# Performance work log

Hardware: AMD Instinct MI355X
Metric: run time of the kernel (lower is better)

## Reference

```python
import jax, jax.numpy as jnp
import numpy as np

B, C, H, W = 8, 512, 32, 32
MID = 64  # in_ch // k = 512 // 8
BN_EPS = 1e-5


def conv1x1(x, Wt, b):
    # x: [B,C,H,W], Wt: [O,C], b: [O]
    return jnp.einsum('bchw,oc->bohw', x, Wt) + b[None, :, None, None]


def batchnorm(x, gamma, beta):
    # train-mode BN: batch statistics over (B,H,W)
    mu = jnp.mean(x, axis=(0, 2, 3), keepdims=True)
    var = jnp.var(x, axis=(0, 2, 3), keepdims=True)
    xn = (x - mu) * jax.lax.rsqrt(var + BN_EPS)
    return xn * gamma[None, :, None, None] + beta[None, :, None, None]


def setup_inputs() -> dict:
    key = jax.random.key(0)
    ks = jax.random.split(key, 8)
    scale = 1.0 / np.sqrt(C)
    x = jax.random.normal(ks[0], (B, C, H, W), dtype=jnp.float32)
    Wf = jax.random.normal(ks[1], (MID, C), dtype=jnp.float32) * scale
    Wg = jax.random.normal(ks[2], (MID, C), dtype=jnp.float32) * scale
    Wh = jax.random.normal(ks[3], (MID, C), dtype=jnp.float32) * scale
    Wv = jax.random.normal(ks[4], (C, MID), dtype=jnp.float32) * (1.0 / np.sqrt(MID))
    return {
        'x': x,
        'Wf': Wf, 'bf': jnp.zeros((MID,), jnp.float32),
        'gamma_f': jnp.ones((MID,), jnp.float32), 'beta_f': jnp.zeros((MID,), jnp.float32),
        'Wg': Wg, 'bg': jnp.zeros((MID,), jnp.float32),
        'gamma_g': jnp.ones((MID,), jnp.float32), 'beta_g': jnp.zeros((MID,), jnp.float32),
        'Wh': Wh, 'bh': jnp.zeros((MID,), jnp.float32),
        'Wv': Wv, 'bv': jnp.zeros((C,), jnp.float32),
    }


def reference(x, Wf, bf, gamma_f, beta_f, Wg, bg, gamma_g, beta_g, Wh, bh, Wv, bv):
    b, c, h, w = x.shape
    hw = h * w
    f_x = jax.nn.relu(batchnorm(conv1x1(x, Wf, bf), gamma_f, beta_f)).reshape(b, MID, hw)
    g_x = jax.nn.relu(batchnorm(conv1x1(x, Wg, bg), gamma_g, beta_g)).reshape(b, MID, hw)
    h_x = conv1x1(x, Wh, bh).reshape(b, MID, hw)
    # z = f_x^T @ g_x : [B, HW, HW]
    z = jnp.einsum('bcn,bcm->bnm', f_x, g_x)
    # spectral normalization by the top singular value
    S = jnp.linalg.svd(z, compute_uv=False)  # sorted descending
    sigma = S[:, 0][:, None, None]
    attn = z / sigma
    # attn @ h_x^T -> [B, HW, MID], then permute to [B, MID, H, W]
    z2 = jnp.einsum('bnm,bcm->bcn', attn, h_x).reshape(b, MID, h, w)
    return conv1x1(z2, Wv, bv) + x
```

## Files before the change

kernel.cpp:

```cpp
#include <hip/hip_runtime.h>

#define B_   8
#define C_   512
#define HW_  1024
#define NCOL (B_*HW_)
#define NROWS 192
#define EPS  1e-5f
#define NCHUNK 32

#define YOFF   0
#define YSZ    (NROWS*NCOL)
#define SPOFF  (YOFF+YSZ)
#define SPSZ   256
#define SP2OFF (SPOFF+SPSZ)
#define SP2SZ  (256*256)
#define CPOFF  (SP2OFF+SP2SZ)
#define CPSZ   (24*NCHUNK*4096)
#define CMOFF  (CPOFF+CPSZ)
#define CMSZ   (24*4096)
#define ISOFF  (CMOFF+CMSZ)
#define UOFF   (ISOFF+16)

typedef unsigned short u16;
typedef __attribute__((ext_vector_type(8))) short short8;
typedef __attribute__((ext_vector_type(4))) float f32x4;

__device__ __forceinline__ u16 f2bf(float f) {
  unsigned u = __float_as_uint(f);
  unsigned r = u + 0x7fffu + ((u >> 16) & 1u);
  return (u16)(r >> 16);
}
__device__ __forceinline__ float bf2f(u16 h) {
  return __uint_as_float(((unsigned)h) << 16);
}
__device__ __forceinline__ void wsplit8(const float* p, short8& hi, short8& lo) {
  #pragma unroll
  for (int i = 0; i < 8; ++i) {
    const float v = p[i];
    const unsigned u = __float_as_uint(v);
    const u16 h = (u16)(u >> 16);
    const float r = v - __uint_as_float(((unsigned)h) << 16);
    const u16 l = (u16)(__float_as_uint(r) >> 16);
    hi[i] = (short)h; lo[i] = (short)l;
  }
}
#define MFMA_B16(a,b,c) __builtin_amdgcn_mfma_f32_16x16x32_bf16(a,b,c,0,0,0)

#define FMA16(a, bb) \
  acc[0][0]+=a.x*bb.x; acc[0][1]+=a.x*bb.y; acc[0][2]+=a.x*bb.z; acc[0][3]+=a.x*bb.w; \
  acc[1][0]+=a.y*bb.x; acc[1][1]+=a.y*bb.y; acc[1][2]+=a.y*bb.z; acc[1][3]+=a.y*bb.w; \
  acc[2][0]+=a.z*bb.x; acc[2][1]+=a.z*bb.y; acc[2][2]+=a.z*bb.z; acc[2][3]+=a.z*bb.w; \
  acc[3][0]+=a.w*bb.x; acc[3][1]+=a.w*bb.y; acc[3][2]+=a.w*bb.z; acc[3][3]+=a.w*bb.w;

__global__ __launch_bounds__(256) void k_conv(
    const float* __restrict__ x,
    const float* __restrict__ Wf, const float* __restrict__ Wg, const float* __restrict__ Wh,
    const float* __restrict__ bf, const float* __restrict__ bg, const float* __restrict__ bh,
    float* __restrict__ ws)
{
  __shared__ u16 Xh[8*32*8];
  __shared__ u16 Xl[8*32*8];
  const int bid = blockIdx.x;
  const int n0  = bid * 32;
  const int b   = n0 >> 10;
  const int hw0 = n0 & 1023;
  const int t   = threadIdx.x;
  const int lane = t & 63;
  const int wid  = t >> 6;
  const int wrow0 = wid * 48;
  const int cst = t & 31, kg2 = t >> 5;
  const int lm = lane & 15, lk = lane >> 4;

  const float* Wrow[3];
  #pragma unroll
  for (int mt = 0; mt < 3; ++mt) {
    const int row = wrow0 + mt*16 + lm;
    Wrow[mt] = (row < 64)  ? Wf + (size_t)row*C_
             : (row < 128) ? Wg + (size_t)(row-64)*C_
             :               Wh + (size_t)(row-128)*C_;
  }

  f32x4 acc[3][2];
  #pragma unroll
  for (int i=0;i<3;++i) { acc[i][0]=(f32x4)0.f; acc[i][1]=(f32x4)0.f; }

  for (int j = 0; j < 8; ++j) {
    const int kk = j*64;
    __syncthreads();
    {
      const float* xp = x + ((size_t)(b*C_ + kk + kg2*8))*HW_ + hw0 + cst;
      u16 hb[8], lb[8];
      #pragma unroll
      for (int i=0;i<8;++i) {
        const float v = xp[(size_t)i*HW_];
        hb[i] = f2bf(v); lb[i] = f2bf(v - bf2f(hb[i]));
      }
      uint4 ph, pl;
      ph.x=(unsigned)hb[0]|((unsigned)hb[1]<<16); ph.y=(unsigned)hb[2]|((unsigned)hb[3]<<16);
      ph.z=(unsigned)hb[4]|((unsigned)hb[5]<<16); ph.w=(unsigned)hb[6]|((unsigned)hb[7]<<16);
      pl.x=(unsigned)lb[0]|((unsigned)lb[1]<<16); pl.y=(unsigned)lb[2]|((unsigned)lb[3]<<16);
      pl.z=(unsigned)lb[4]|((unsigned)lb[5]<<16); pl.w=(unsigned)lb[6]|((unsigned)lb[7]<<16);
      *reinterpret_cast<uint4*>(&Xh[(kg2*32+cst)*8]) = ph;
      *reinterpret_cast<uint4*>(&Xl[(kg2*32+cst)*8]) = pl;
    }
    __syncthreads();
    #pragma unroll
    for (int kb = 0; kb < 2; ++kb) {
      short8 bhf[2], blf[2];
      #pragma unroll
      for (int nt = 0; nt < 2; ++nt) {
        const int col = nt*16 + lm;
        const int idx = ((kb*4 + lk)*32 + col)*8;
        bhf[nt] = *reinterpret_cast<const short8*>(&Xh[idx]);
        blf[nt] = *reinterpret_cast<const short8*>(&Xl[idx]);
      }
      #pragma unroll
      for (int mt = 0; mt < 3; ++mt) {
        float wv[8];
        *reinterpret_cast<float4*>(&wv[0]) = *reinterpret_cast<const float4*>(&Wrow[mt][kk + kb*32 + lk*8]);
        *reinterpret_cast<float4*>(&wv[4]) = *reinterpret_cast<const float4*>(&Wrow[mt][kk + kb*32 + lk*8 + 4]);
        short8 ah, al;
        wsplit8(wv, ah, al);
        #pragma unroll
        for (int nt = 0; nt < 2; ++nt) {
          acc[mt][nt] = MFMA_B16(ah, bhf[nt], acc[mt][nt]);
          acc[mt][nt] = MFMA_B16(al, bhf[nt], acc[mt][nt]);
          acc[mt][nt] = MFMA_B16(ah, blf[nt], acc[mt][nt]);
        }
      }
    }
  }
  #pragma unroll
  for (int mt = 0; mt < 3; ++mt) {
    const int rbase = wrow0 + mt*16;
    const float* bp = (rbase < 64) ? bf : (rbase < 128) ? bg : bh;
    const int rloc0 = (rbase & 63) + lk*4;
    #pragma unroll
    for (int r = 0; r < 4; ++r) {
      const int row = rbase + lk*4 + r;
      const float bi = bp[rloc0 + r];
      const float y0 = acc[mt][0][r] + bi;
      const float y1 = acc[mt][1][r] + bi;
      ws[YOFF + (size_t)row*NCOL + n0 + lm]      = y0;
      ws[YOFF + (size_t)row*NCOL + n0 + 16 + lm] = y1;
      if (rbase < 128) {
        float s  = y0 + y1;
        float s2 = y0*y0 + y1*y1;
        #pragma unroll
        for (int off = 1; off < 16; off <<= 1) {
          s  += __shfl_xor(s,  off);
          s2 += __shfl_xor(s2, off);
        }
        if (lm == 0) {
          ws[SP2OFF + bid*256 + row*2 + 0] = s;
          ws[SP2OFF + bid*256 + row*2 + 1] = s2;
        }
      }
    }
  }
}

__global__ __launch_bounds__(256) void k_cpart(
    const float* __restrict__ gamma_f, const float* __restrict__ beta_f,
    const float* __restrict__ gamma_g, const float* __restrict__ beta_g,
    float* __restrict__ ws)
{
  __shared__ u16 Sh[3][64][40];
  __shared__ u16 Sl[3][64][40];
  __shared__ float tot[256];
  __shared__ float scs[128], sfs[128];
  const int chunk = blockIdx.x, b = blockIdx.y;
  const int t = threadIdx.x;

  {
    float s = 0.f;
    const float* sp = ws + SP2OFF + t;
    #pragma unroll 8
    for (int blk = 0; blk < 256; ++blk) s += sp[blk*256];
    tot[t] = s;
  }
  __syncthreads();
  if (t < 128) {
    const float s = tot[t*2], s2 = tot[t*2+1];
    const float mean = s*(1.0f/NCOL);
    const float var  = s2*(1.0f/NCOL) - mean*mean;
    const float g  = (t < 64) ? gamma_f[t] : gamma_g[t-64];
    const float be = (t < 64) ? beta_f[t]  : beta_g[t-64];
    const float sc = g * rsqrtf(var + EPS);
    const float sf = be - mean*sc;
    scs[t] = sc; sfs[t] = sf;
    if (chunk == 0 && b == 0) {
      const int jj = (t < 64) ? t : t + 64;
      ws[SPOFF + jj]      = sc;
      ws[SPOFF + jj + 64] = sf;
    }
  }
  __syncthreads();

  const int bcol0 = b*1024 + chunk*32;
  for (int q = t; q < 1536; q += 256) {
    const int mm = q >> 9, rem = q & 511;
    const int r = rem >> 3, c4 = (rem & 7) * 4;
    const float4 v = *reinterpret_cast<const float4*>(
        &ws[YOFF + (size_t)(mm*64 + r)*NCOL + bcol0 + c4]);
    float v0, v1, v2, v3;
    if (mm < 2) {
      const float sc = scs[mm*64 + r], sf = sfs[mm*64 + r];
      v0 = fmaxf(sc*v.x+sf, 0.f); v1 = fmaxf(sc*v.y+sf, 0.f);
      v2 = fmaxf(sc*v.z+sf, 0.f); v3 = fmaxf(sc*v.w+sf, 0.f);
    } else { v0=v.x; v1=v.y; v2=v.z; v3=v.w; }
    const u16 h0=f2bf(v0), h1=f2bf(v1), h2=f2bf(v2), h3=f2bf(v3);
    uint2 ph; ph.x=(unsigned)h0|((unsigned)h1<<16); ph.y=(unsigned)h2|((unsigned)h3<<16);
    uint2 pl;
    pl.x=(unsigned)f2bf(v0-bf2f(h0)) | ((unsigned)f2bf(v1-bf2f(h1))<<16);
    pl.y=(unsigned)f2bf(v2-bf2f(h2)) | ((unsigned)f2bf(v3-bf2f(h3))<<16);
    *reinterpret_cast<uint2*>(&Sh[mm][r][c4]) = ph;
    *reinterpret_cast<uint2*>(&Sl[mm][r][c4]) = pl;
  }
  __syncthreads();
  {
    const int lane = t & 63, wid = t >> 6;
    const int lm = lane & 15, lk = lane >> 4;
    const int mt0 = (wid >> 1)*2, nt0 = (wid & 1)*2;
    const int ko = lk*8;
    short8 ah[3][2], al[3][2];
    #pragma unroll
    for (int m = 0; m < 3; ++m)
      #pragma unroll
      for (int mi = 0; mi < 2; ++mi) {
        const int row = (mt0+mi)*16 + lm;
        ah[m][mi] = *reinterpret_cast<const short8*>(&Sh[m][row][ko]);
        al[m][mi] = *reinterpret_cast<const short8*>(&Sl[m][row][ko]);
      }
    short8 bhf[2][2], blf[2][2];
    #pragma unroll
    for (int m = 0; m < 2; ++m)
      #pragma unroll
      for (int ni = 0; ni < 2; ++ni) {
        const int row = (nt0+ni)*16 + lm;
        bhf[m][ni] = *reinterpret_cast<const short8*>(&Sh[m][row][ko]);
        blf[m][ni] = *reinterpret_cast<const short8*>(&Sl[m][row][ko]);
      }
    f32x4 acc2[3][2][2];
    #pragma unroll
    for (int p=0;p<3;++p) for (int i=0;i<2;++i) for (int j=0;j<2;++j) acc2[p][i][j]=(f32x4)0.f;
    #pragma unroll
    for (int p = 0; p < 3; ++p) {
      const int am = p;
      const int bm = (p==0) ? 0 : 1;
      #pragma unroll
      for (int mi = 0; mi < 2; ++mi)
        #pragma unroll
        for (int ni = 0; ni < 2; ++ni) {
          acc2[p][mi][ni] = MFMA_B16(ah[am][mi], bhf[bm][ni], acc2[p][mi][ni]);
          acc2[p][mi][ni] = MFMA_B16(al[am][mi], bhf[bm][ni], acc2[p][mi][ni]);
          acc2[p][mi][ni] = MFMA_B16(ah[am][mi], blf[bm][ni], acc2[p][mi][ni]);
        }
    }
    float* cp = ws + CPOFF;
    #pragma unroll
    for (int p = 0; p < 3; ++p) {
      float* base = cp + ((size_t)((b*3+p)*NCHUNK + chunk))*4096;
      #pragma unroll
      for (int mi = 0; mi < 2; ++mi)
        #pragma unroll
        for (int ni = 0; ni < 2; ++ni) {
          const int col = (nt0+ni)*16 + lm;
          #pragma unroll
          for (int r = 0; r < 4; ++r) {
            const int row = (mt0+mi)*16 + lk*4 + r;
            base[(size_t)row*64 + col] = acc2[p][mi][ni][r];
          }
        }
    }
  }
}

__global__ __launch_bounds__(256) void k_creduce(float* __restrict__ ws)
{
  const int m = blockIdx.y;
  const int q = blockIdx.x*256 + threadIdx.x;
  const float4* src = reinterpret_cast<const float4*>(ws + CPOFF) + (size_t)m*NCHUNK*1024;
  float4 s = {0.f,0.f,0.f,0.f};
  #pragma unroll 8
  for (int ch = 0; ch < NCHUNK; ++ch) {
    const float4 p = src[(size_t)ch*1024 + q];
    s.x+=p.x; s.y+=p.y; s.z+=p.z; s.w+=p.w;
  }
  *(reinterpret_cast<float4*>(ws + CMOFF) + (size_t)m*1024 + q) = s;
}

__global__ __launch_bounds__(256) void k_su(const float* __restrict__ Wv, float* __restrict__ ws)
{
  __shared__ float smA[64][64];
  __shared__ float smB[64][64];
  const int bid = blockIdx.x;
  const int t = threadIdx.x;
  if (bid < 64) {
    const int b = bid >> 3, rt = bid & 7;
    const float* T = ws + CMOFF + (size_t)(b*3+2)*4096;
    for (int q = t; q < 1024; q += 256)
      *(reinterpret_cast<float4*>(&smB[0][0]) + q) = *(reinterpret_cast<const float4*>(T) + q);
    for (int q = t; q < 1024; q += 256) {
      const int row = q >> 4;
      const int c4  = (q & 15) * 4;
      const float4 wv = *reinterpret_cast<const float4*>(&Wv[(size_t)(rt*64+row)*64 + c4]);
      smA[c4+0][row]=wv.x; smA[c4+1][row]=wv.y; smA[c4+2][row]=wv.z; smA[c4+3][row]=wv.w;
    }
    __syncthreads();
    const int ti = t >> 4, tj = t & 15;
    float acc[4][4] = {};
    #pragma unroll
    for (int c = 0; c < 64; ++c) {
      const float4 a  = *reinterpret_cast<const float4*>(&smA[c][ti*4]);
      const float4 bb = *reinterpret_cast<const float4*>(&smB[c][tj*4]);
      FMA16(a, bb)
    }
    #pragma unroll
    for (int i = 0; i < 4; ++i) {
      float4 o; o.x = acc[i][0]; o.y = acc[i][1]; o.z = acc[i][2]; o.w = acc[i][3];
      *reinterpret_cast<float4*>(&ws[UOFF + ((size_t)b*512 + rt*64 + ti*4+i)*64 + tj*4]) = o;
    }
  } else {
    const int b = bid - 64;
    float* vsh = &smA[0][0];
    float* ush = &smA[1][0];
    const float* Cf = ws + CMOFF + (size_t)(b*3+0)*4096;
    const float* Cg = ws + CMOFF + (size_t)(b*3+1)*4096;
    float cfr[64], cgr[64];
    if (t < 64) {
      #pragma unroll
      for (int k4 = 0; k4 < 16; ++k4) {
        const float4 fa = *reinterpret_cast<const float4*>(&Cf[t*64 + k4*4]);
        const float4 fc = *reinterpret_cast<const float4*>(&Cg[t*64 + k4*4]);
        cfr[k4*4+0]=fa.x; cfr[k4*4+1]=fa.y; cfr[k4*4+2]=fa.z; cfr[k4*4+3]=fa.w;
        cgr[k4*4+0]=fc.x; cgr[k4*4+1]=fc.y; cgr[k4*4+2]=fc.z; cgr[k4*4+3]=fc.w;
      }
    }
    float vloc = 0.125f;
    if (t < 64) vsh[t] = vloc;
    __syncthreads();
    const int NIT = 16;
    float lambda = 0.f;
    for (int it = 0; it <= NIT; ++it) {
      if (t < 64) {
        float u0=0.f,u1=0.f,u2=0.f,u3=0.f;
        #pragma unroll
        for (int j4 = 0; j4 < 16; ++j4) {
          const float4 vq = *reinterpret_cast<const float4*>(&vsh[j4*4]);
          u0 += cfr[j4*4+0]*vq.x; u1 += cfr[j4*4+1]*vq.y;
          u2 += cfr[j4*4+2]*vq.z; u3 += cfr[j4*4+3]*vq.w;
        }
        ush[t] = (u0+u1)+(u2+u3);
      }
      __syncthreads();
      float w = 0.f;
      if (t < 64) {
        float w0=0.f,w1=0.f,w2=0.f,w3=0.f;
        #pragma unroll
        for (int j4 = 0; j4 < 16; ++j4) {
          const float4 uq = *reinterpret_cast<const float4*>(&ush[j4*4]);
          w0 += cgr[j4*4+0]*uq.x; w1 += cgr[j4*4+1]*uq.y;
          w2 += cgr[j4*4+2]*uq.z; w3 += cgr[j4*4+3]*uq.w;
        }
        w = (w0+w1)+(w2+w3);
      }
      if (it == NIT) {
        if (t < 64) {
          float num = vloc * w;
          #pragma unroll
          for (int off = 32; off > 0; off >>= 1) num += __shfl_xor(num, off);
          lambda = num;
        }
      } else {
        if (t < 64) {
          float n2 = w*w;
          #pragma unroll
          for (int off = 32; off > 0; off >>= 1) n2 += __shfl_xor(n2, off);
          const float rn = rsqrtf(fmaxf(n2, 1e-30f));
          vloc = w * rn;
        }
        __syncthreads();
        if (t < 64) vsh[t] = vloc;
        __syncthreads();
      }
    }
    if (t == 0) ws[ISOFF + b] = rsqrtf(fmaxf(lambda, 1e-30f));
  }
}

__global__ __launch_bounds__(256) void k_final(
    const float* __restrict__ x, const float* __restrict__ bv,
    float* __restrict__ out, const float* __restrict__ ws)
{
  __shared__ float Ut[64][64];
  __shared__ float Fl[64][64];
  __shared__ float scF[64], sfF[64];
  const int nt = blockIdx.x, ot = blockIdx.y, b = blockIdx.z;
  const int t = threadIdx.x;
  if (t < 64) {
    scF[t] = ws[SPOFF + t];
    sfF[t] = ws[SPOFF + 64 + t];
  }
  for (int q = t; q < 1024; q += 256) {
    const int row = q >> 4, k4 = (q & 15)*4;
    const float4 uv = *reinterpret_cast<const float4*>(
        &ws[UOFF + ((size_t)b*512 + ot*64 + row)*64 + k4]);
    Ut[k4+0][row]=uv.x; Ut[k4+1][row]=uv.y; Ut[k4+2][row]=uv.z; Ut[k4+3][row]=uv.w;
  }
  for (int q = t; q < 1024; q += 256) {
    const int k = q >> 4, c4 = (q & 15)*4;
    const float4 yv = *reinterpret_cast<const float4*>(
        &ws[YOFF + (size_t)k*NCOL + b*1024 + nt*64 + c4]);
    Fl[k][c4+0]=yv.x; Fl[k][c4+1]=yv.y; Fl[k][c4+2]=yv.z; Fl[k][c4+3]=yv.w;
  }
  __syncthreads();
  for (int q = t; q < 1024; q += 256) {
    const int k = q >> 4, c4 = (q & 15)*4;
    const float s = scF[k], f = sfF[k];
    Fl[k][c4+0]=fmaxf(s*Fl[k][c4+0]+f,0.f); Fl[k][c4+1]=fmaxf(s*Fl[k][c4+1]+f,0.f);
    Fl[k][c4+2]=fmaxf(s*Fl[k][c4+2]+f,0.f); Fl[k][c4+3]=fmaxf(s*Fl[k][c4+3]+f,0.f);
  }
  __syncthreads();
  const float isig = ws[ISOFF + b];
  const int ti = t >> 4, tj = t & 15;
  float acc[4][4] = {};
  #pragma unroll
  for (int k = 0; k < 64; ++k) {
    const float4 a  = *reinterpret_cast<const float4*>(&Ut[k][ti*4]);
    const float4 bb = *reinterpret_cast<const float4*>(&Fl[k][tj*4]);
    FMA16(a, bb)
  }
  #pragma unroll
  for (int i = 0; i < 4; ++i) {
    const int oc = ot*64 + ti*4 + i;
    const float bvv = bv[oc];
    const size_t base = ((size_t)b*C_ + oc)*HW_ + nt*64 + tj*4;
    const float4 xv = *reinterpret_cast<const float4*>(&x[base]);
    float4 o;
    o.x = acc[i][0]*isig+bvv+xv.x; o.y = acc[i][1]*isig+bvv+xv.y;
    o.z = acc[i][2]*isig+bvv+xv.z; o.w = acc[i][3]*isig+bvv+xv.w;
    *reinterpret_cast<float4*>(&out[base]) = o;
  }
}

extern "C" void kernel_launch(void* const* d_in, const int* in_sizes, int n_in,
                              void* d_out, int out_size, void* d_ws, size_t ws_size,
                              hipStream_t stream) {
  (void)in_sizes; (void)n_in; (void)out_size; (void)ws_size;
  const float* x       = (const float*)d_in[0];
  const float* Wf      = (const float*)d_in[1];
  const float* bf      = (const float*)d_in[2];
  const float* gamma_f = (const float*)d_in[3];
  const float* beta_f  = (const float*)d_in[4];
  const float* Wg      = (const float*)d_in[5];
  const float* bg      = (const float*)d_in[6];
  const float* gamma_g = (const float*)d_in[7];
  const float* beta_g  = (const float*)d_in[8];
  const float* Wh      = (const float*)d_in[9];
  const float* bh      = (const float*)d_in[10];
  const float* Wv      = (const float*)d_in[11];
  const float* bv      = (const float*)d_in[12];
  float* out = (float*)d_out;
  float* ws  = (float*)d_ws;

  k_conv   <<<256,             256, 0, stream>>>(x, Wf, Wg, Wh, bf, bg, bh, ws);
  k_cpart  <<<dim3(NCHUNK,8),  256, 0, stream>>>(gamma_f, beta_f, gamma_g, beta_g, ws);
  k_creduce<<<dim3(4,24),      256, 0, stream>>>(ws);
  k_su     <<<72,              256, 0, stream>>>(Wv, ws);
  k_final  <<<dim3(16,8,8),    256, 0, stream>>>(x, bv, out, ws);
}
```

Baseline: 86.58 us.

## Pre-split conv weights once, prefetch x into registers, fold chunk reduction into k_su

A new k_prep kernel splits the f/g/h weights into bf16 hi/lo arrays once, so k_conv loads ready bf16 fragments instead of redoing the split in every block. k_conv now loads all 64 x values per thread into registers up front, so global loads are issued early rather than inside the loop. The k_creduce launch is removed, and k_su sums the 32 partial chunks itself into padded shared memory. This trades one extra small launch for one fewer launch, at the cost of more register pressure in k_conv and redundant partial-sum reads across the 8 row-tile blocks per batch in k_su.

```diff
diff --git a/kernel.cpp b/kernel.cpp
--- a/kernel.cpp
+++ b/kernel.cpp
@@ -14,11 +14,11 @@
 #define SPSZ   256
 #define SP2OFF (SPOFF+SPSZ)
 #define SP2SZ  (256*256)
-#define CPOFF  (SP2OFF+SP2SZ)
+#define WOFF   (SP2OFF+SP2SZ)
+#define WSZ    98304
+#define CPOFF  (WOFF+WSZ)
 #define CPSZ   (24*NCHUNK*4096)
-#define CMOFF  (CPOFF+CPSZ)
-#define CMSZ   (24*4096)
-#define ISOFF  (CMOFF+CMSZ)
+#define ISOFF  (CPOFF+CPSZ)
 #define UOFF   (ISOFF+16)
 
 typedef unsigned short u16;
@@ -32,17 +32,6 @@
 }
 __device__ __forceinline__ float bf2f(u16 h) {
   return __uint_as_float(((unsigned)h) << 16);
-}
-__device__ __forceinline__ void wsplit8(const float* p, short8& hi, short8& lo) {
-  #pragma unroll
-  for (int i = 0; i < 8; ++i) {
-    const float v = p[i];
-    const unsigned u = __float_as_uint(v);
-    const u16 h = (u16)(u >> 16);
-    const float r = v - __uint_as_float(((unsigned)h) << 16);
-    const u16 l = (u16)(__float_as_uint(r) >> 16);
-    hi[i] = (short)h; lo[i] = (short)l;
-  }
 }
 #define MFMA_B16(a,b,c) __builtin_amdgcn_mfma_f32_16x16x32_bf16(a,b,c,0,0,0)
 
@@ -52,14 +41,36 @@
   acc[2][0]+=a.z*bb.x; acc[2][1]+=a.z*bb.y; acc[2][2]+=a.z*bb.z; acc[2][3]+=a.z*bb.w; \
   acc[3][0]+=a.w*bb.x; acc[3][1]+=a.w*bb.y; acc[3][2]+=a.w*bb.z; acc[3][3]+=a.w*bb.w;
 
+__global__ __launch_bounds__(256) void k_prep(
+    const float* __restrict__ Wf, const float* __restrict__ Wg,
+    const float* __restrict__ Wh, float* __restrict__ ws)
+{
+  u16* Whi = (u16*)(ws + WOFF);
+  u16* Wlo = Whi + NROWS*C_;
+  const int e4 = blockIdx.x*256 + threadIdx.x;
+  const int e  = e4*4;
+  const int row = e >> 9, k = e & 511;
+  const float* src = (row < 64) ? &Wf[row*C_ + k]
+                   : (row < 128) ? &Wg[(row-64)*C_ + k]
+                   : &Wh[(row-128)*C_ + k];
+  const float4 v = *reinterpret_cast<const float4*>(src);
+  u16 h0=f2bf(v.x), h1=f2bf(v.y), h2=f2bf(v.z), h3=f2bf(v.w);
+  u16 l0=f2bf(v.x-bf2f(h0)), l1=f2bf(v.y-bf2f(h1)), l2=f2bf(v.z-bf2f(h2)), l3=f2bf(v.w-bf2f(h3));
+  uint2 ph; ph.x = (unsigned)h0 | ((unsigned)h1<<16); ph.y = (unsigned)h2 | ((unsigned)h3<<16);
+  uint2 pl; pl.x = (unsigned)l0 | ((unsigned)l1<<16); pl.y = (unsigned)l2 | ((unsigned)l3<<16);
+  *reinterpret_cast<uint2*>(&Whi[e]) = ph;
+  *reinterpret_cast<uint2*>(&Wlo[e]) = pl;
+}
+
 __global__ __launch_bounds__(256) void k_conv(
     const float* __restrict__ x,
-    const float* __restrict__ Wf, const float* __restrict__ Wg, const float* __restrict__ Wh,
     const float* __restrict__ bf, const float* __restrict__ bg, const float* __restrict__ bh,
     float* __restrict__ ws)
 {
   __shared__ u16 Xh[8*32*8];
   __shared__ u16 Xl[8*32*8];
+  const u16* Whi = (const u16*)(ws + WOFF);
+  const u16* Wlo = Whi + NROWS*C_;
   const int bid = blockIdx.x;
   const int n0  = bid * 32;
   const int b   = n0 >> 10;
@@ -71,28 +82,29 @@
   const int cst = t & 31, kg2 = t >> 5;
   const int lm = lane & 15, lk = lane >> 4;
 
-  const float* Wrow[3];
-  #pragma unroll
-  for (int mt = 0; mt < 3; ++mt) {
-    const int row = wrow0 + mt*16 + lm;
-    Wrow[mt] = (row < 64)  ? Wf + (size_t)row*C_
-             : (row < 128) ? Wg + (size_t)(row-64)*C_
-             :               Wh + (size_t)(row-128)*C_;
+  float xr[64];
+  {
+    const float* xp = x + ((size_t)(b*C_ + kg2*8))*HW_ + hw0 + cst;
+    #pragma unroll
+    for (int j = 0; j < 8; ++j)
+      #pragma unroll
+      for (int i = 0; i < 8; ++i)
+        xr[j*8+i] = xp[(size_t)(j*64 + i)*HW_];
   }
 
   f32x4 acc[3][2];
   #pragma unroll
   for (int i=0;i<3;++i) { acc[i][0]=(f32x4)0.f; acc[i][1]=(f32x4)0.f; }
 
+  #pragma unroll
   for (int j = 0; j < 8; ++j) {
     const int kk = j*64;
     __syncthreads();
     {
-      const float* xp = x + ((size_t)(b*C_ + kk + kg2*8))*HW_ + hw0 + cst;
       u16 hb[8], lb[8];
       #pragma unroll
       for (int i=0;i<8;++i) {
-        const float v = xp[(size_t)i*HW_];
+        const float v = xr[j*8+i];
         hb[i] = f2bf(v); lb[i] = f2bf(v - bf2f(hb[i]));
       }
       uint4 ph, pl;
@@ -116,11 +128,10 @@
       }
       #pragma unroll
       for (int mt = 0; mt < 3; ++mt) {
-        float wv[8];
-        *reinterpret_cast<float4*>(&wv[0]) = *reinterpret_cast<const float4*>(&Wrow[mt][kk + kb*32 + lk*8]);
-        *reinterpret_cast<float4*>(&wv[4]) = *reinterpret_cast<const float4*>(&Wrow[mt][kk + kb*32 + lk*8 + 4]);
-        short8 ah, al;
-        wsplit8(wv, ah, al);
+        const int row = wrow0 + mt*16 + lm;
+        const size_t widx = (size_t)row*C_ + kk + kb*32 + lk*8;
+        const short8 ah = *reinterpret_cast<const short8*>(&Whi[widx]);
+        const short8 al = *reinterpret_cast<const short8*>(&Wlo[widx]);
         #pragma unroll
         for (int nt = 0; nt < 2; ++nt) {
           acc[mt][nt] = MFMA_B16(ah, bhf[nt], acc[mt][nt]);
@@ -276,31 +287,27 @@
   }
 }
 
-__global__ __launch_bounds__(256) void k_creduce(float* __restrict__ ws)
-{
-  const int m = blockIdx.y;
-  const int q = blockIdx.x*256 + threadIdx.x;
-  const float4* src = reinterpret_cast<const float4*>(ws + CPOFF) + (size_t)m*NCHUNK*1024;
-  float4 s = {0.f,0.f,0.f,0.f};
-  #pragma unroll 8
-  for (int ch = 0; ch < NCHUNK; ++ch) {
-    const float4 p = src[(size_t)ch*1024 + q];
-    s.x+=p.x; s.y+=p.y; s.z+=p.z; s.w+=p.w;
-  }
-  *(reinterpret_cast<float4*>(ws + CMOFF) + (size_t)m*1024 + q) = s;
-}
-
 __global__ __launch_bounds__(256) void k_su(const float* __restrict__ Wv, float* __restrict__ ws)
 {
-  __shared__ float smA[64][64];
-  __shared__ float smB[64][64];
+  __shared__ float smA[64][68];
+  __shared__ float smB[64][68];
+  __shared__ float vsh[64], ush[64];
   const int bid = blockIdx.x;
   const int t = threadIdx.x;
+  const float4* cp4 = reinterpret_cast<const float4*>(ws + CPOFF);
+
   if (bid < 64) {
     const int b = bid >> 3, rt = bid & 7;
-    const float* T = ws + CMOFF + (size_t)(b*3+2)*4096;
-    for (int q = t; q < 1024; q += 256)
-      *(reinterpret_cast<float4*>(&smB[0][0]) + q) = *(reinterpret_cast<const float4*>(T) + q);
+    const float4* TP = cp4 + (size_t)((b*3+2)*NCHUNK)*1024;
+    for (int q = t; q < 1024; q += 256) {
+      float4 s = {0.f,0.f,0.f,0.f};
+      #pragma unroll 8
+      for (int ch = 0; ch < NCHUNK; ++ch) {
+        const float4 p = TP[(size_t)ch*1024 + q];
+        s.x+=p.x; s.y+=p.y; s.z+=p.z; s.w+=p.w;
+      }
+      *reinterpret_cast<float4*>(&smB[q >> 4][(q & 15)*4]) = s;
+    }
     for (int q = t; q < 1024; q += 256) {
       const int row = q >> 4;
       const int c4  = (q & 15) * 4;
@@ -323,16 +330,27 @@
     }
   } else {
     const int b = bid - 64;
-    float* vsh = &smA[0][0];
-    float* ush = &smA[1][0];
-    const float* Cf = ws + CMOFF + (size_t)(b*3+0)*4096;
-    const float* Cg = ws + CMOFF + (size_t)(b*3+1)*4096;
+    const float4* CfP = cp4 + (size_t)((b*3+0)*NCHUNK)*1024;
+    const float4* CgP = cp4 + (size_t)((b*3+1)*NCHUNK)*1024;
+    for (int q = t; q < 1024; q += 256) {
+      float4 sa = {0.f,0.f,0.f,0.f}, sb = {0.f,0.f,0.f,0.f};
+      #pragma unroll 8
+      for (int ch = 0; ch < NCHUNK; ++ch) {
+        const float4 pa = CfP[(size_t)ch*1024 + q];
+        const float4 pb = CgP[(size_t)ch*1024 + q];
+        sa.x+=pa.x; sa.y+=pa.y; sa.z+=pa.z; sa.w+=pa.w;
+        sb.x+=pb.x; sb.y+=pb.y; sb.z+=pb.z; sb.w+=pb.w;
+      }
+      *reinterpret_cast<float4*>(&smA[q >> 4][(q & 15)*4]) = sa;
+      *reinterpret_cast<float4*>(&smB[q >> 4][(q & 15)*4]) = sb;
+    }
+    __syncthreads();
     float cfr[64], cgr[64];
     if (t < 64) {
       #pragma unroll
       for (int k4 = 0; k4 < 16; ++k4) {
-        const float4 fa = *reinterpret_cast<const float4*>(&Cf[t*64 + k4*4]);
-        const float4 fc = *reinterpret_cast<const float4*>(&Cg[t*64 + k4*4]);
+        const float4 fa = *reinterpret_cast<const float4*>(&smA[t][k4*4]);
+        const float4 fc = *reinterpret_cast<const float4*>(&smB[t][k4*4]);
         cfr[k4*4+0]=fa.x; cfr[k4*4+1]=fa.y; cfr[k4*4+2]=fa.z; cfr[k4*4+3]=fa.w;
         cgr[k4*4+0]=fc.x; cgr[k4*4+1]=fc.y; cgr[k4*4+2]=fc.z; cgr[k4*4+3]=fc.w;
       }
@@ -464,9 +482,9 @@
   float* out = (float*)d_out;
   float* ws  = (float*)d_ws;
 
-  k_conv   <<<256,             256, 0, stream>>>(x, Wf, Wg, Wh, bf, bg, bh, ws);
-  k_cpart  <<<dim3(NCHUNK,8),  256, 0, stream>>>(gamma_f, beta_f, gamma_g, beta_g, ws);
-  k_creduce<<<dim3(4,24),      256, 0, stream>>>(ws);
-  k_su     <<<72,              256, 0, stream>>>(Wv, ws);
-  k_final  <<<dim3(16,8,8),    256, 0, stream>>>(x, bv, out, ws);
-}
+  k_prep <<<96,             256, 0, stream>>>(Wf, Wg, Wh, ws);
+  k_conv <<<256,            256, 0, stream>>>(x, bf, bg, bh, ws);
+  k_cpart<<<dim3(NCHUNK,8), 256, 0, stream>>>(gamma_f, beta_f, gamma_g, beta_g, ws);
+  k_su   <<<72,             256, 0, stream>>>(Wv, ws);
+  k_final<<<dim3(16,8,8),   256, 0, stream>>>(x, bv, out, ws);
+}
```

Result: slower. 94.63 us (+9.3%).
